# Performance work log

Hardware: AMD Instinct MI355X
Metric: run time of the kernel (lower is better)

## Reference

```python
import jax, jax.numpy as jnp
import numpy as np

# FP4 E2M1 representable magnitudes and midpoints for round-to-nearest
FP4_GRID = jnp.array([0.0, 0.5, 1.0, 1.5, 2.0, 3.0, 4.0, 6.0], dtype=jnp.float32)
FP4_MIDS = jnp.array([0.25, 0.75, 1.25, 1.75, 2.5, 3.5, 5.0], dtype=jnp.float32)
FP4_MAX = 6.0


def fp4_fake_quant(x):
    """Per-tensor absmax-scaled FP4 (E2M1) fake quantization with STE."""
    scale = jnp.maximum(jnp.max(jnp.abs(x)) / FP4_MAX, 1e-12)
    y = x / scale
    sign = jnp.sign(y)
    mag = jnp.minimum(jnp.abs(y), FP4_MAX)
    idx = jnp.searchsorted(FP4_MIDS, mag)  # round-to-nearest FP4 magnitude
    q = FP4_GRID[idx] * sign * scale
    # straight-through estimator: identity gradient through quantization
    return x + jax.lax.stop_gradient(q - x)


def setup_inputs() -> dict:
    key = jax.random.key(0)
    k1, k2 = jax.random.split(key)
    x = jax.random.normal(k1, (8192, 4096), dtype=jnp.float32)
    weight = jax.random.normal(k2, (4096, 4096), dtype=jnp.float32)
    bias = jnp.zeros((4096,), dtype=jnp.float32)
    return {"x": x, "weight": weight, "bias": bias}


def reference(x, weight, bias):
    # FP4-quantized linear: quantize activations and weights, then GEMM + bias
    xq = fp4_fake_quant(x)            # [T, in]
    wq = fp4_fake_quant(weight)       # [in, out]
    return xq @ wq + bias             # [T, out]
```

## Files before the change

### kernel.cpp

```cpp
#include <hip/hip_runtime.h>
#include <hip/hip_bf16.h>

typedef __attribute__((ext_vector_type(8))) __bf16 bf16x8;
typedef __attribute__((ext_vector_type(4))) float f32x4;

__device__ __forceinline__ unsigned short fp4_q_bf16(float x, float scale) {
    float mag = fabsf(x) / scale;
    float g = mag > 2.5f ? (mag > 5.0f ? 6.0f : (mag > 3.5f ? 4.0f : 3.0f))
                         : (mag > 1.25f ? (mag > 1.75f ? 2.0f : 1.5f)
                                        : (mag > 0.75f ? 1.0f
                                                       : (mag > 0.25f ? 0.5f : 0.0f)));
    unsigned gb = __float_as_uint(g) >> 16;
    unsigned sb = (__float_as_uint(x) >> 16) & 0x8000u;
    return (unsigned short)(gb | sb);
}

__device__ __forceinline__ float load_scale(const unsigned* amax_bits) {
    float am = __uint_as_float(*amax_bits);
    return fmaxf(am / 6.0f, 1e-12f);
}

__global__ void absmax_kernel(const float4* __restrict__ in, long long n4,
                              unsigned* __restrict__ out) {
    float m = 0.0f;
    long long stride = (long long)gridDim.x * blockDim.x;
    for (long long i = (long long)blockIdx.x * blockDim.x + threadIdx.x; i < n4; i += stride) {
        float4 v = in[i];
        m = fmaxf(m, fmaxf(fmaxf(fabsf(v.x), fabsf(v.y)), fmaxf(fabsf(v.z), fabsf(v.w))));
    }
    #pragma unroll
    for (int off = 32; off > 0; off >>= 1)
        m = fmaxf(m, __shfl_xor(m, off));
    if ((threadIdx.x & 63) == 0)
        atomicMax(out, __float_as_uint(m));
}

__global__ void quant_kernel(const float4* __restrict__ in,
                             const unsigned* __restrict__ amax_bits,
                             ushort4* __restrict__ out, long long n4) {
    float scale = load_scale(amax_bits);
    long long stride = (long long)gridDim.x * blockDim.x;
    for (long long i = (long long)blockIdx.x * blockDim.x + threadIdx.x; i < n4; i += stride) {
        float4 v = in[i];
        ushort4 o;
        o.x = fp4_q_bf16(v.x, scale);
        o.y = fp4_q_bf16(v.y, scale);
        o.z = fp4_q_bf16(v.z, scale);
        o.w = fp4_q_bf16(v.w, scale);
        out[i] = o;
    }
}

__global__ __launch_bounds__(256)
void quant_w_t_kernel(const float* __restrict__ w,
                      const unsigned* __restrict__ amax_bits,
                      unsigned short* __restrict__ wqT, int N, int K) {
    __shared__ unsigned short tile[64][65];
    float scale = load_scale(amax_bits);
    int t = threadIdx.x;
    int bk = blockIdx.x;
    int bn = blockIdx.y;
    int r0 = t >> 4;
    int c4 = (t & 15) * 4;
    #pragma unroll
    for (int i = 0; i < 4; ++i) {
        int r = r0 + i * 16;
        float4 v = *(const float4*)&w[(size_t)(bk * 64 + r) * N + bn * 64 + c4];
        tile[r][c4 + 0] = fp4_q_bf16(v.x, scale);
        tile[r][c4 + 1] = fp4_q_bf16(v.y, scale);
        tile[r][c4 + 2] = fp4_q_bf16(v.z, scale);
        tile[r][c4 + 3] = fp4_q_bf16(v.w, scale);
    }
    __syncthreads();
    #pragma unroll
    for (int i = 0; i < 4; ++i) {
        int rr = r0 + i * 16;
        ushort4 o;
        o.x = tile[c4 + 0][rr];
        o.y = tile[c4 + 1][rr];
        o.z = tile[c4 + 2][rr];
        o.w = tile[c4 + 3][rr];
        *(ushort4*)&wqT[(size_t)(bn * 64 + rr) * K + bk * 64 + c4] = o;
    }
}

__device__ __forceinline__ void gload_lds16(const unsigned short* g, unsigned short* l) {
    __builtin_amdgcn_global_load_lds(
        (const __attribute__((address_space(1))) unsigned int*)g,
        (__attribute__((address_space(3))) unsigned int*)l, 16, 0, 0);
}

__global__ __launch_bounds__(256)
void gemm_kernel(const unsigned short* __restrict__ A,
                 const unsigned short* __restrict__ B,
                 const unsigned* __restrict__ amax_bits,
                 const float* __restrict__ bias,
                 float* __restrict__ C, int M, int N, int K) {
    __shared__ unsigned short As[128 * 64];
    __shared__ unsigned short Bs[128 * 64];

    int tid  = threadIdx.x;
    int wave = tid >> 6;
    int lane = tid & 63;

    int nbn = N >> 7;
    int bx  = blockIdx.x;
    int cpx = gridDim.x >> 3;
    int swz = (bx & 7) * cpx + (bx >> 3);
    int bm  = swz / nbn;
    int bn  = swz % nbn;

    float sx  = load_scale(amax_bits + 0);
    float sw  = load_scale(amax_bits + 1);
    float sxw = sx * sw;

    int wrow = wave >> 1;
    int wcol = wave & 1;
    int lrow = lane >> 3;
    int slot = lane & 7;
    int sswz = slot ^ lrow;

    size_t a_base = (size_t)(bm * 128) * K;
    size_t b_base = (size_t)(bn * 128) * K;

    int l15 = lane & 15;
    int l4  = lane >> 4;
    int r7  = lane & 7;

    f32x4 acc[4][4] = {};

    for (int kt = 0; kt < K; kt += 64) {
        #pragma unroll
        for (int i = 0; i < 4; ++i) {
            int chunk = wave * 4 + i;
            int row   = chunk * 8 + lrow;
            size_t go = (size_t)row * K + kt + sswz * 8;
            gload_lds16(A + a_base + go, &As[chunk * 512]);
            gload_lds16(B + b_base + go, &Bs[chunk * 512]);
        }
        __syncthreads();

        #pragma unroll
        for (int kk = 0; kk < 2; ++kk) {
            bf16x8 af[4], bfr[4];
            #pragma unroll
            for (int mi = 0; mi < 4; ++mi) {
                int row = wrow * 64 + mi * 16 + l15;
                int sl  = (kk * 4 + l4) ^ r7;
                af[mi] = *(const bf16x8*)&As[row * 64 + sl * 8];
            }
            #pragma unroll
            for (int ni = 0; ni < 4; ++ni) {
                int row = wcol * 64 + ni * 16 + l15;
                int sl  = (kk * 4 + l4) ^ r7;
                bfr[ni] = *(const bf16x8*)&Bs[row * 64 + sl * 8];
            }
            #pragma unroll
            for (int mi = 0; mi < 4; ++mi)
                #pragma unroll
                for (int ni = 0; ni < 4; ++ni)
                    acc[mi][ni] = __builtin_amdgcn_mfma_f32_16x16x32_bf16(
                        af[mi], bfr[ni], acc[mi][ni], 0, 0, 0);
        }
        __syncthreads();
    }

    int r0 = bm * 128 + wrow * 64;
    int c0 = bn * 128 + wcol * 64;
    #pragma unroll
    for (int ni = 0; ni < 4; ++ni) {
        int col = c0 + ni * 16 + l15;
        float bv = bias[col];
        #pragma unroll
        for (int mi = 0; mi < 4; ++mi) {
            int rbase = r0 + mi * 16 + l4 * 4;
            #pragma unroll
            for (int j = 0; j < 4; ++j)
                C[(size_t)(rbase + j) * N + col] = acc[mi][ni][j] * sxw + bv;
        }
    }
}

extern "C" void kernel_launch(void* const* d_in, const int* in_sizes, int n_in,
                              void* d_out, int out_size, void* d_ws, size_t ws_size,
                              hipStream_t stream) {
    const float* x    = (const float*)d_in[0];
    const float* w    = (const float*)d_in[1];
    const float* bias = (const float*)d_in[2];
    float* out        = (float*)d_out;

    int N = in_sizes[2];
    int K = in_sizes[1] / N;
    int M = in_sizes[0] / K;

    unsigned* amax        = (unsigned*)d_ws;
    unsigned short* xq    = (unsigned short*)((char*)d_ws + 256);
    unsigned short* wqT   = (unsigned short*)((char*)xq + (size_t)M * K * 2);

    hipMemsetAsync(d_ws, 0, 256, stream);

    long long nx4 = (long long)M * K / 4;
    long long nw4 = (long long)K * N / 4;

    absmax_kernel<<<1024, 256, 0, stream>>>((const float4*)x, nx4, amax + 0);
    absmax_kernel<<<1024, 256, 0, stream>>>((const float4*)w, nw4, amax + 1);

    quant_kernel<<<2048, 256, 0, stream>>>((const float4*)x, amax + 0, (ushort4*)xq, nx4);
    quant_w_t_kernel<<<dim3(K / 64, N / 64), 256, 0, stream>>>(w, amax + 1, wqT, N, K);

    dim3 grid((M / 128) * (N / 128));
    gemm_kernel<<<grid, 256, 0, stream>>>(xq, wqT, amax, bias, out, M, N, K);
}
```

Baseline: 780.1 us.

## Replace GEMM with double-buffered 256x256 tile, 8-wave kernel with prefetch

The 128x128 single-buffered GEMM becomes a 256x256 tile kernel with 512 threads and 128 KB of double-buffered LDS. The next K-tile is loaded asynchronously into the other buffer while the current one feeds the MFMAs, with fine-grained barriers and setprio to interleave loads and math. The larger tile raises data reuse per byte loaded. In exchange it needs much more LDS and registers per block, uses only 512 blocks, and launch_bounds(512,2) may not fit two blocks per CU.

```diff
diff --git a/kernel.cpp b/kernel.cpp
--- a/kernel.cpp
+++ b/kernel.cpp
@@ -58,8 +58,7 @@
     __shared__ unsigned short tile[64][65];
     float scale = load_scale(amax_bits);
     int t = threadIdx.x;
-    int bk = blockIdx.x;
-    int bn = blockIdx.y;
+    int bk = blockIdx.x, bn = blockIdx.y;
     int r0 = t >> 4;
     int c4 = (t & 15) * 4;
     #pragma unroll
@@ -90,89 +89,123 @@
         (__attribute__((address_space(3))) unsigned int*)l, 16, 0, 0);
 }
 
-__global__ __launch_bounds__(256)
-void gemm_kernel(const unsigned short* __restrict__ A,
-                 const unsigned short* __restrict__ B,
-                 const unsigned* __restrict__ amax_bits,
-                 const float* __restrict__ bias,
-                 float* __restrict__ C, int M, int N, int K) {
-    __shared__ unsigned short As[128 * 64];
-    __shared__ unsigned short Bs[128 * 64];
-
-    int tid  = threadIdx.x;
-    int wave = tid >> 6;
-    int lane = tid & 63;
-
-    int nbn = N >> 7;
-    int bx  = blockIdx.x;
+__device__ __forceinline__ void stage_op(const unsigned short* __restrict__ G,
+                                         unsigned short* lbase, int K,
+                                         int kt, int j4, int wave, int lane) {
+    int rloc = j4 * 64 + wave * 8;
+    int row  = rloc + (lane >> 3);
+    int slot = (lane & 7) ^ (lane >> 3);
+    size_t go = (size_t)row * K + kt + slot * 8;
+    gload_lds16(G + go, lbase + (size_t)rloc * 64);
+}
+
+__global__ __launch_bounds__(512, 2)
+void gemm256_kernel(const unsigned short* __restrict__ A,
+                    const unsigned short* __restrict__ B,
+                    const unsigned* __restrict__ amax_bits,
+                    const float* __restrict__ bias,
+                    float* __restrict__ C, int M, int N, int K) {
+    __shared__ unsigned short smem[65536];
+
+    int tid = threadIdx.x;
+    int wave = tid >> 6, lane = tid & 63;
+    int wr = wave >> 2, wc = wave & 3;
+    int l15 = lane & 15, l4 = lane >> 4, l7 = lane & 7;
+
+    int nbn = N >> 8;
     int cpx = gridDim.x >> 3;
-    int swz = (bx & 7) * cpx + (bx >> 3);
-    int bm  = swz / nbn;
-    int bn  = swz % nbn;
-
-    float sx  = load_scale(amax_bits + 0);
-    float sw  = load_scale(amax_bits + 1);
-    float sxw = sx * sw;
-
-    int wrow = wave >> 1;
-    int wcol = wave & 1;
-    int lrow = lane >> 3;
-    int slot = lane & 7;
-    int sswz = slot ^ lrow;
-
-    size_t a_base = (size_t)(bm * 128) * K;
-    size_t b_base = (size_t)(bn * 128) * K;
-
-    int l15 = lane & 15;
-    int l4  = lane >> 4;
-    int r7  = lane & 7;
-
-    f32x4 acc[4][4] = {};
-
-    for (int kt = 0; kt < K; kt += 64) {
+    int swz = ((int)blockIdx.x & 7) * cpx + ((int)blockIdx.x >> 3);
+    int bm = swz / nbn, bn = swz % nbn;
+
+    float sxw = load_scale(amax_bits + 0) * load_scale(amax_bits + 1);
+
+    const unsigned short* Ag = A + (size_t)(bm * 256) * K;
+    const unsigned short* Bg = B + (size_t)(bn * 256) * K;
+
+    #pragma unroll
+    for (int j4 = 0; j4 < 4; ++j4) stage_op(Ag, smem,         K, 0, j4, wave, lane);
+    #pragma unroll
+    for (int j4 = 0; j4 < 4; ++j4) stage_op(Bg, smem + 16384, K, 0, j4, wave, lane);
+    asm volatile("s_waitcnt vmcnt(0)" ::: "memory");
+    __builtin_amdgcn_s_barrier();
+
+    f32x4 acc[8][4] = {};
+    int NT = K >> 6;
+    int cur = 0;
+
+    for (int t = 0; t < NT; ++t) {
+        unsigned short* As_ = smem + cur * 32768;
+        unsigned short* Bs_ = As_ + 16384;
+        unsigned short* An_ = smem + (cur ^ 1) * 32768;
+        unsigned short* Bn_ = An_ + 16384;
+        int ktn = (t + 1) << 6;
+        bool pf = (t + 1 < NT);
+
+        bf16x8 bfrag[2][4];
+
         #pragma unroll
-        for (int i = 0; i < 4; ++i) {
-            int chunk = wave * 4 + i;
-            int row   = chunk * 8 + lrow;
-            size_t go = (size_t)row * K + kt + sswz * 8;
-            gload_lds16(A + a_base + go, &As[chunk * 512]);
-            gload_lds16(B + b_base + go, &Bs[chunk * 512]);
+        for (int q = 0; q < 4; ++q) {
+            bf16x8 afrag[2][2];
+            #pragma unroll
+            for (int s = 0; s < 2; ++s) {
+                int row = wr * 128 + (2 * q + s) * 16 + l15;
+                #pragma unroll
+                for (int kk = 0; kk < 2; ++kk) {
+                    int slot = (kk * 4 + l4) ^ l7;
+                    afrag[kk][s] = *(const bf16x8*)&As_[row * 64 + slot * 8];
+                }
+            }
+            if (q == 0) {
+                #pragma unroll
+                for (int ni = 0; ni < 4; ++ni) {
+                    int row = wc * 64 + ni * 16 + l15;
+                    #pragma unroll
+                    for (int kk = 0; kk < 2; ++kk) {
+                        int slot = (kk * 4 + l4) ^ l7;
+                        bfrag[kk][ni] = *(const bf16x8*)&Bs_[row * 64 + slot * 8];
+                    }
+                }
+                if (pf) {
+                    #pragma unroll
+                    for (int j4 = 0; j4 < 4; ++j4)
+                        stage_op(Ag, An_, K, ktn, j4, wave, lane);
+                }
+            }
+            if (q == 1 && pf) {
+                #pragma unroll
+                for (int j4 = 0; j4 < 4; ++j4)
+                    stage_op(Bg, Bn_, K, ktn, j4, wave, lane);
+            }
+
+            __builtin_amdgcn_s_barrier();
+            asm volatile("s_waitcnt lgkmcnt(0)" ::: "memory");
+            __builtin_amdgcn_sched_barrier(0);
+            __builtin_amdgcn_s_setprio(1);
+            #pragma unroll
+            for (int kk = 0; kk < 2; ++kk)
+                #pragma unroll
+                for (int s = 0; s < 2; ++s)
+                    #pragma unroll
+                    for (int ni = 0; ni < 4; ++ni)
+                        acc[2 * q + s][ni] = __builtin_amdgcn_mfma_f32_16x16x32_bf16(
+                            afrag[kk][s], bfrag[kk][ni], acc[2 * q + s][ni], 0, 0, 0);
+            __builtin_amdgcn_s_setprio(0);
+            if (q == 3) {
+                asm volatile("s_waitcnt vmcnt(0)" ::: "memory");
+            }
+            __builtin_amdgcn_s_barrier();
         }
-        __syncthreads();
-
-        #pragma unroll
-        for (int kk = 0; kk < 2; ++kk) {
-            bf16x8 af[4], bfr[4];
-            #pragma unroll
-            for (int mi = 0; mi < 4; ++mi) {
-                int row = wrow * 64 + mi * 16 + l15;
-                int sl  = (kk * 4 + l4) ^ r7;
-                af[mi] = *(const bf16x8*)&As[row * 64 + sl * 8];
-            }
-            #pragma unroll
-            for (int ni = 0; ni < 4; ++ni) {
-                int row = wcol * 64 + ni * 16 + l15;
-                int sl  = (kk * 4 + l4) ^ r7;
-                bfr[ni] = *(const bf16x8*)&Bs[row * 64 + sl * 8];
-            }
-            #pragma unroll
-            for (int mi = 0; mi < 4; ++mi)
-                #pragma unroll
-                for (int ni = 0; ni < 4; ++ni)
-                    acc[mi][ni] = __builtin_amdgcn_mfma_f32_16x16x32_bf16(
-                        af[mi], bfr[ni], acc[mi][ni], 0, 0, 0);
-        }
-        __syncthreads();
-    }
-
-    int r0 = bm * 128 + wrow * 64;
-    int c0 = bn * 128 + wcol * 64;
+        cur ^= 1;
+    }
+
+    int r0 = bm * 256 + wr * 128;
+    int c0 = bn * 256 + wc * 64;
     #pragma unroll
     for (int ni = 0; ni < 4; ++ni) {
         int col = c0 + ni * 16 + l15;
         float bv = bias[col];
         #pragma unroll
-        for (int mi = 0; mi < 4; ++mi) {
+        for (int mi = 0; mi < 8; ++mi) {
             int rbase = r0 + mi * 16 + l4 * 4;
             #pragma unroll
             for (int j = 0; j < 4; ++j)
@@ -193,9 +226,9 @@
     int K = in_sizes[1] / N;
     int M = in_sizes[0] / K;
 
-    unsigned* amax        = (unsigned*)d_ws;
-    unsigned short* xq    = (unsigned short*)((char*)d_ws + 256);
-    unsigned short* wqT   = (unsigned short*)((char*)xq + (size_t)M * K * 2);
+    unsigned* amax      = (unsigned*)d_ws;
+    unsigned short* xq  = (unsigned short*)((char*)d_ws + 256);
+    unsigned short* wqT = (unsigned short*)((char*)xq + (size_t)M * K * 2);
 
     hipMemsetAsync(d_ws, 0, 256, stream);
 
@@ -208,6 +241,6 @@
     quant_kernel<<<2048, 256, 0, stream>>>((const float4*)x, amax + 0, (ushort4*)xq, nx4);
     quant_w_t_kernel<<<dim3(K / 64, N / 64), 256, 0, stream>>>(w, amax + 1, wqT, N, K);
 
-    dim3 grid((M / 128) * (N / 128));
-    gemm_kernel<<<grid, 256, 0, stream>>>(xq, wqT, amax, bias, out, M, N, K);
-}
+    dim3 grid((M / 256) * (N / 256));
+    gemm256_kernel<<<grid, 512, 0, stream>>>(xq, wqT, amax, bias, out, M, N, K);
+}
```

New measurement: 631.5 us. -19.1%, faster.
